# Kernel optimization log

Measured on AMD Instinct MI355X. Metric: run time of the kernel, lower is better.

## Reference

```python
import jax, jax.numpy as jnp
import numpy as np

N_NODES = 100000
N_EDGES = 1600000
F_IN, H1, H2, N_CLS = 512, 180, 120, 40
NEG_SLOPE = 0.01  # F.leaky_relu default


def setup_inputs() -> dict:
    key = jax.random.key(0)
    ks = jax.random.split(key, 8)
    x = jax.random.normal(ks[0], (N_NODES, F_IN), dtype=jnp.float32)
    edge_index = jax.random.randint(ks[1], (2, N_EDGES), 0, N_NODES, dtype=jnp.int64)
    W1 = jax.random.normal(ks[2], (F_IN, H1), dtype=jnp.float32) / np.sqrt(F_IN)
    b1 = jnp.zeros((H1,), dtype=jnp.float32)
    W2 = jax.random.normal(ks[3], (H1, H2), dtype=jnp.float32) / np.sqrt(H1)
    b2 = jnp.zeros((H2,), dtype=jnp.float32)
    W3 = jax.random.normal(ks[4], (H2, N_CLS), dtype=jnp.float32) / np.sqrt(H2)
    b3 = jnp.zeros((N_CLS,), dtype=jnp.float32)
    return {"x": x, "edge_index": edge_index, "W1": W1, "b1": b1,
            "W2": W2, "b2": b2, "W3": W3, "b3": b3}


def _add_self_loops(edge_index, n):
    loop = jnp.arange(n, dtype=edge_index.dtype)
    src = jnp.concatenate([edge_index[0], loop])
    dst = jnp.concatenate([edge_index[1], loop])
    return src, dst


def _gcn_conv(h, src, dst, norm, W, b, n):
    # PyG GCNConv: linear transform first, then normalized scatter-add at dst.
    h = h @ W  # [N, out]
    msg = norm[:, None] * h[src]  # gather at source, per-edge scale
    out = jax.ops.segment_sum(msg, dst, num_segments=n)  # scatter-add at dest
    return out + b


def reference(x, edge_index, W1, b1, W2, b2, W3, b3):
    n = x.shape[0]
    src, dst = _add_self_loops(edge_index, n)
    # symmetric normalization deg^-1/2 * deg^-1/2 on self-loop-augmented graph
    ones = jnp.ones(dst.shape[0], dtype=x.dtype)
    deg = jax.ops.segment_sum(ones, dst, num_segments=n)
    dinv = jnp.where(deg > 0, jax.lax.rsqrt(deg), 0.0)
    norm = dinv[src] * dinv[dst]  # [E+N]

    h = _gcn_conv(x, src, dst, norm, W1, b1, n)
    h = jnp.where(h >= 0, h, NEG_SLOPE * h)
    h = _gcn_conv(h, src, dst, norm, W2, b2, n)
    h = jnp.where(h >= 0, h, NEG_SLOPE * h)
    logits = h @ W3 + b3
    return jax.nn.log_softmax(logits, axis=1)
```

## Files before the change

### kernel.cpp

```cpp
#include <hip/hip_runtime.h>
#include <math.h>

typedef __attribute__((ext_vector_type(8))) short short8;
typedef __attribute__((ext_vector_type(4))) float f32x4;

static constexpr int F_IN = 512;
static constexpr int H1V = 180, H1P = 192;
static constexpr int H2V = 120, H2P = 128;
static constexpr int NC  = 40,  NCP = 64;

__device__ inline unsigned f2bf(float f) {
    unsigned u = __float_as_uint(f);
    return (u + 0x7fffu + ((u >> 16) & 1u)) >> 16;
}
__device__ inline unsigned cvtpk(float lo, float hi) {
    unsigned r;
    asm("v_cvt_pk_bf16_f32 %0, %1, %2" : "=v"(r) : "v"(lo), "v"(hi));
    return r;
}
#define BLO(u) __uint_as_float((u) << 16)
#define BHI(u) __uint_as_float((u) & 0xffff0000u)

__device__ inline void gload_lds16(const void* gsrc, void* ldst) {
    __builtin_amdgcn_global_load_lds(
        (const __attribute__((address_space(1))) void*)gsrc,
        (__attribute__((address_space(3))) void*)ldst, 16, 0, 0);
}

__global__ void k_init(const int* __restrict__ ei, int* __restrict__ flag,
                       const float* __restrict__ W1, const float* __restrict__ W2,
                       const float* __restrict__ W3, const float* __restrict__ b1,
                       const float* __restrict__ b2, const float* __restrict__ b3,
                       unsigned short* __restrict__ W1s, unsigned short* __restrict__ W2s,
                       unsigned short* __restrict__ W3s, float* __restrict__ b1p,
                       float* __restrict__ b2p, float* __restrict__ b3p) {
    if (blockIdx.x < 16) {
        int i = blockIdx.x * 256 + threadIdx.x;
        if (ei[2 * i + 1] != 0) flag[0] = 1;
        return;
    }
    const int n1 = F_IN * H1P;
    const int n2 = n1 + H1P * H2P;
    const int n3 = n2 + H2P * NCP;
    const int n4 = n3 + H1P;
    const int n5 = n4 + H2P;
    const int n6 = n5 + NCP;
    int i = (blockIdx.x - 16) * 256 + threadIdx.x;
    if (i < n1) {
        int k = i / H1P, c = i % H1P;
        float v = (c < H1V) ? W1[k * H1V + c] : 0.0f;
        W1s[(size_t)(k >> 3) * H1P * 8 + c * 8 + (k & 7)] = (unsigned short)f2bf(v);
    } else if (i < n2) {
        int j = i - n1;
        int k = j / H2P, c = j % H2P;
        float v = (k < H1V && c < H2V) ? W2[k * H2V + c] : 0.0f;
        W2s[(size_t)(k >> 3) * H2P * 8 + c * 8 + (k & 7)] = (unsigned short)f2bf(v);
    } else if (i < n3) {
        int j = i - n2;
        int k = j / NCP, c = j % NCP;
        float v = (k < H2V && c < NC) ? W3[k * NC + c] : 0.0f;
        W3s[(size_t)(k >> 3) * NCP * 8 + c * 8 + (k & 7)] = (unsigned short)f2bf(v);
    } else if (i < n4) {
        int c = i - n3;
        b1p[c] = (c < H1V) ? b1[c] : 0.0f;
    } else if (i < n5) {
        int c = i - n4;
        b2p[c] = (c < H2V) ? b2[c] : 0.0f;
    } else if (i < n6) {
        int c = i - n5;
        b3p[c] = (c < NC) ? b3[c] : -1e30f;
    }
}

__global__ void k_hist(const int* __restrict__ ei, int E, const int* __restrict__ flag,
                       int* __restrict__ deg, int* __restrict__ dst32,
                       uint2* __restrict__ sr) {
    int e = blockIdx.x * 256 + threadIdx.x;
    if (e >= E) return;
    bool i64 = (flag[0] == 0);
    int s, d;
    if (i64) { s = ei[2 * e]; d = ei[2 * E + 2 * e]; }
    else     { s = ei[e];     d = ei[E + e]; }
    int r = atomicAdd(&deg[d], 1);
    dst32[e] = d;
    sr[e] = make_uint2((unsigned)s, (unsigned)r);
}

__global__ void k_scan1(const int* __restrict__ deg, int* __restrict__ rp,
                        int* __restrict__ bsum, float* __restrict__ dinv, int n) {
    __shared__ int s[256];
    int t = threadIdx.x;
    int base = blockIdx.x * 1024 + t * 4;
    int v0 = (base + 0 < n) ? deg[base + 0] : 0;
    int v1 = (base + 1 < n) ? deg[base + 1] : 0;
    int v2 = (base + 2 < n) ? deg[base + 2] : 0;
    int v3 = (base + 3 < n) ? deg[base + 3] : 0;
    if (base + 0 < n) dinv[base + 0] = rsqrtf((float)(v0 + 1));
    if (base + 1 < n) dinv[base + 1] = rsqrtf((float)(v1 + 1));
    if (base + 2 < n) dinv[base + 2] = rsqrtf((float)(v2 + 1));
    if (base + 3 < n) dinv[base + 3] = rsqrtf((float)(v3 + 1));
    int sum = v0 + v1 + v2 + v3;
    s[t] = sum;
    __syncthreads();
    for (int off = 1; off < 256; off <<= 1) {
        int x = (t >= off) ? s[t - off] : 0;
        __syncthreads();
        s[t] += x;
        __syncthreads();
    }
    int run = s[t] - sum;
    if (t == 255) bsum[blockIdx.x] = s[255];
    if (base + 0 < n) rp[base + 0] = run; run += v0;
    if (base + 1 < n) rp[base + 1] = run; run += v1;
    if (base + 2 < n) rp[base + 2] = run; run += v2;
    if (base + 3 < n) rp[base + 3] = run;
}

__global__ void k_scan2(int* __restrict__ bsum, int nb) {
    __shared__ int s[128];
    int t = threadIdx.x;
    int v = (t < nb) ? bsum[t] : 0;
    s[t] = v;
    __syncthreads();
    for (int off = 1; off < 128; off <<= 1) {
        int x = (t >= off) ? s[t - off] : 0;
        __syncthreads();
        s[t] += x;
        __syncthreads();
    }
    if (t < nb) bsum[t] = s[t] - v;
}

__global__ void k_scan3(const int* __restrict__ bsum, int* __restrict__ rp,
                        int n, int E) {
    int i = blockIdx.x * 256 + threadIdx.x;
    if (i < n) {
        rp[i] = rp[i] + bsum[i >> 10];
    } else if (i == n) {
        rp[n] = E;
    }
}

__global__ __launch_bounds__(256) void k_fill(const int* __restrict__ dst32,
                                              const uint2* __restrict__ sr, int E,
                                              const int* __restrict__ rp,
                                              int* __restrict__ csr,
                                              int bw, int chunk) {
    int bkt = blockIdx.x & 7;
    int lo = bkt * bw, hi = lo + bw;
    int ch = blockIdx.x >> 3;
    int e0 = ch * chunk;
    int e1 = min(E, e0 + chunk);
    for (int e = e0 + (int)threadIdx.x; e < e1; e += 256) {
        int d = dst32[e];
        if (d >= lo && d < hi) {
            uint2 v = sr[e];
            csr[rp[d] + (int)v.y] = (int)v.x;
        }
    }
}

__global__ __launch_bounds__(256) void k_gemm1(const float* __restrict__ X,
                                               const short8* __restrict__ Bs,
                                               const float* __restrict__ dinv,
                                               signed char* __restrict__ Hq,
                                               float* __restrict__ sc,
                                               int M) {
    __shared__ float ldsf[6144];
    char* lds = (char*)ldsf;
    int t = threadIdx.x;
    int w = t >> 6, l = t & 63;
    int lr = l & 15, kg = l >> 4;
    int row0 = blockIdx.x * 32;
    int colb = w * 48;

    f32x4 acc[2][3];
#pragma unroll
    for (int m = 0; m < 2; ++m)
#pragma unroll
        for (int nn = 0; nn < 3; ++nn) acc[m][nn] = (f32x4){0.f, 0.f, 0.f, 0.f};

    auto stage = [&](int kb, int buf) {
#pragma unroll
        for (int j = 0; j < 2; ++j) {
            int o = j * 4096 + t * 16;
            int row = o >> 8;
            int col4 = ((o >> 4) & 15) ^ (row & 15);
            int rowg = row0 + row;
            if (rowg >= M) rowg = M - 1;
            gload_lds16(X + (size_t)rowg * F_IN + kb + col4 * 4,
                        lds + buf * 8192 + j * 4096 + w * 1024);
        }
    };

    short8 breg[2][2][3];
    auto loadB = [&](int ts, int pp) {
#pragma unroll
        for (int kk = 0; kk < 2; ++kk)
#pragma unroll
            for (int nn = 0; nn < 3; ++nn)
                breg[pp][kk][nn] =
                    Bs[(size_t)(ts * 8 + kk * 4 + kg) * H1P + colb + nn * 16 + lr];
    };

    auto compute = [&](int cur, int pp) {
#pragma unroll
        for (int kk = 0; kk < 2; ++kk) {
            short8 a[2];
#pragma unroll
            for (int m = 0; m < 2; ++m) {
                int row = m * 16 + lr;
                char* base = lds + cur * 8192 + row * 256;
                int c0 = kk * 8 + kg * 2;
                float4 v0 = *(const float4*)(base + (((c0 + 0) ^ (row & 15)) * 16));
                float4 v1 = *(const float4*)(base + (((c0 + 1) ^ (row & 15)) * 16));
                union { unsigned u[4]; short8 s; } cu;
                cu.u[0] = cvtpk(v0.x, v0.y);
                cu.u[1] = cvtpk(v0.z, v0.w);
                cu.u[2] = cvtpk(v1.x, v1.y);
                cu.u[3] = cvtpk(v1.z, v1.w);
                a[m] = cu.s;
            }
#pragma unroll
            for (int m = 0; m < 2; ++m)
#pragma unroll
                for (int nn = 0; nn < 3; ++nn)
                    acc[m][nn] = __builtin_amdgcn_mfma_f32_16x16x32_bf16(
                        a[m], breg[pp][kk][nn], acc[m][nn], 0, 0, 0);
        }
    };

    stage(0, 0);
    stage(64, 1);
    loadB(0, 0);
    asm volatile("s_waitcnt vmcnt(8)" ::: "memory");
    __builtin_amdgcn_s_barrier();
    __builtin_amdgcn_sched_barrier(0);

#pragma unroll
    for (int ts = 0; ts < 8; ++ts) {
        if (ts < 6) stage((ts + 2) * 64, (ts + 2) % 3);
        if (ts < 7) loadB(ts + 1, (ts + 1) & 1);
        compute(ts % 3, ts & 1);
        if (ts < 7) {
            if (ts < 6) {
                asm volatile("s_waitcnt vmcnt(8)" ::: "memory");
            } else {
                asm volatile("s_waitcnt vmcnt(6)" ::: "memory");
            }
            __builtin_amdgcn_s_barrier();
            __builtin_amdgcn_sched_barrier(0);
        }
    }

    __syncthreads();
    float* rmaxp = (float*)lds;
#pragma unroll
    for (int m = 0; m < 2; ++m) {
#pragma unroll
        for (int j = 0; j < 4; ++j) {
            int rl = m * 16 + kg * 4 + j;
            int grow = row0 + rl;
            float dv = (grow < M) ? dinv[grow] : 0.f;
            float lm = 0.f;
#pragma unroll
            for (int nn = 0; nn < 3; ++nn)
                lm = fmaxf(lm, fabsf(acc[m][nn][j] * dv));
#pragma unroll
            for (int d = 1; d < 16; d <<= 1)
                lm = fmaxf(lm, __shfl_xor(lm, d));
            if (lr == 0) rmaxp[rl * 4 + w] = lm;
        }
    }
    __syncthreads();
#pragma unroll
    for (int m = 0; m < 2; ++m) {
#pragma unroll
        for (int j = 0; j < 4; ++j) {
            int rl = m * 16 + kg * 4 + j;
            int grow = row0 + rl;
            if (grow >= M) continue;
            float dv = dinv[grow];
            float rm = fmaxf(fmaxf(rmaxp[rl * 4 + 0], rmaxp[rl * 4 + 1]),
                             fmaxf(rmaxp[rl * 4 + 2], rmaxp[rl * 4 + 3]));
            float inv = (rm > 0.f) ? 127.0f / rm : 0.f;
            if (w == 0 && lr == 0) sc[grow] = rm * (1.0f / 127.0f);
#pragma unroll
            for (int nn = 0; nn < 3; ++nn) {
                float v = acc[m][nn][j] * dv * inv;
                v = fminf(fmaxf(rintf(v), -127.f), 127.f);
                Hq[(size_t)grow * H1P + colb + nn * 16 + lr] = (signed char)(int)v;
            }
        }
    }
}

__global__ __launch_bounds__(256) void k_gat1q(const signed char* __restrict__ Hq,
                                               const float* __restrict__ sc,
                                               const float* __restrict__ dinv,
                                               const int* __restrict__ rp,
                                               const int* __restrict__ csr,
                                               const float* __restrict__ bias,
                                               uint2* __restrict__ out, int n) {
    int wv = threadIdx.x >> 6, l = threadIdx.x & 63;
    int i = blockIdx.x * 4 + wv;
    if (i >= n) return;
    bool act = l < 48;
    int c = act ? l : 0;
    const unsigned* Hr = (const unsigned*)(Hq + c * 4);

    float a0, a1, a2, a3;
    {
        unsigned w0 = Hr[(size_t)i * 48];
        float s0 = sc[i];
        a0 = (float)(signed char)(w0) * s0;
        a1 = (float)(signed char)(w0 >> 8) * s0;
        a2 = (float)(signed char)(w0 >> 16) * s0;
        a3 = (float)(signed char)(w0 >> 24) * s0;
    }
    float p0 = 0.f, p1 = 0.f, p2 = 0.f, p3 = 0.f;

    int e0 = rp[i], e1 = rp[i + 1];
    int e = e0;
    for (; e + 7 < e1; e += 8) {
        int s[8];
#pragma unroll
        for (int q = 0; q < 8; ++q) s[q] = csr[e + q];
        float scs[8];
#pragma unroll
        for (int q = 0; q < 8; ++q) scs[q] = sc[s[q]];
        unsigned v[8];
#pragma unroll
        for (int q = 0; q < 8; ++q) v[q] = Hr[(size_t)s[q] * 48];
#pragma unroll
        for (int q = 0; q < 8; q += 2) {
            a0 = fmaf((float)(signed char)(v[q]), scs[q], a0);
            a1 = fmaf((float)(signed char)(v[q] >> 8), scs[q], a1);
            a2 = fmaf((float)(signed char)(v[q] >> 16), scs[q], a2);
            a3 = fmaf((float)(signed char)(v[q] >> 24), scs[q], a3);
            p0 = fmaf((float)(signed char)(v[q + 1]), scs[q + 1], p0);
            p1 = fmaf((float)(signed char)(v[q + 1] >> 8), scs[q + 1], p1);
            p2 = fmaf((float)(signed char)(v[q + 1] >> 16), scs[q + 1], p2);
            p3 = fmaf((float)(signed char)(v[q + 1] >> 24), scs[q + 1], p3);
        }
    }
    for (; e < e1; ++e) {
        int s0 = csr[e];
        float sq = sc[s0];
        unsigned w0 = Hr[(size_t)s0 * 48];
        a0 = fmaf((float)(signed char)(w0), sq, a0);
        a1 = fmaf((float)(signed char)(w0 >> 8), sq, a1);
        a2 = fmaf((float)(signed char)(w0 >> 16), sq, a2);
        a3 = fmaf((float)(signed char)(w0 >> 24), sq, a3);
    }
    a0 += p0; a1 += p1; a2 += p2; a3 += p3;

    float di = dinv[i];
    float4 bb = *(const float4*)(bias + 4 * c);
    float o0 = fmaf(di, a0, bb.x);
    float o1 = fmaf(di, a1, bb.y);
    float o2 = fmaf(di, a2, bb.z);
    float o3 = fmaf(di, a3, bb.w);
    o0 = o0 >= 0.f ? o0 : 0.01f * o0;
    o1 = o1 >= 0.f ? o1 : 0.01f * o1;
    o2 = o2 >= 0.f ? o2 : 0.01f * o2;
    o3 = o3 >= 0.f ? o3 : 0.01f * o3;
    if (act) {
        uint2 r;
        r.x = (f2bf(o1) << 16) | f2bf(o0);
        r.y = (f2bf(o3) << 16) | f2bf(o2);
        out[(size_t)i * 48 + c] = r;
    }
}

__global__ __launch_bounds__(512) void k_gemm2(const unsigned short* __restrict__ A,
                                               const short8* __restrict__ Bs,
                                               const float* __restrict__ dinv,
                                               unsigned short* __restrict__ Hout,
                                               int M) {
    __shared__ unsigned short ldsu[16384];
    char* lds = (char*)ldsu;
    int t = threadIdx.x;
    int w = t >> 6, l = t & 63;
    int lr = l & 15, kg = l >> 4;
    int wr = w >> 2, wc = w & 3;
    int row0 = blockIdx.x * 128;
    int colb = wc * 32;

    f32x4 acc[4][2];
#pragma unroll
    for (int m = 0; m < 4; ++m)
#pragma unroll
        for (int nn = 0; nn < 2; ++nn) acc[m][nn] = (f32x4){0.f, 0.f, 0.f, 0.f};

    auto stage = [&](int kb, int buf) {
#pragma unroll
        for (int j = 0; j < 2; ++j) {
            int o = j * 8192 + t * 16;
            int row = o >> 7;
            int chunk = ((o >> 4) & 7) ^ (row & 7);
            int rowg = row0 + row;
            if (rowg >= M) rowg = M - 1;
            gload_lds16(A + (size_t)rowg * H1P + kb + chunk * 8,
                        lds + buf * 16384 + j * 8192 + w * 1024);
        }
    };

    stage(0, 0);
    __syncthreads();

    for (int ts = 0; ts < 3; ++ts) {
        int cur = ts & 1;
        if (ts < 2) stage((ts + 1) * 64, cur ^ 1);
        short8 b[2][2];
#pragma unroll
        for (int kk = 0; kk < 2; ++kk)
#pragma unroll
            for (int nn = 0; nn < 2; ++nn)
                b[kk][nn] = Bs[(size_t)(ts * 8 + kk * 4 + kg) * H2P + colb + nn * 16 + lr];
        short8 a[2][4];
#pragma unroll
        for (int kk = 0; kk < 2; ++kk)
#pragma unroll
            for (int m = 0; m < 4; ++m) {
                int row = wr * 64 + m * 16 + lr;
                a[kk][m] = *(const short8*)(lds + cur * 16384 + row * 128 +
                                            (((kk * 4 + kg) ^ (row & 7)) * 16));
            }
#pragma unroll
        for (int kk = 0; kk < 2; ++kk)
#pragma unroll
            for (int m = 0; m < 4; ++m)
#pragma unroll
                for (int nn = 0; nn < 2; ++nn)
                    acc[m][nn] = __builtin_amdgcn_mfma_f32_16x16x32_bf16(a[kk][m], b[kk][nn], acc[m][nn], 0, 0, 0);
        __syncthreads();
    }

#pragma unroll
    for (int m = 0; m < 4; ++m) {
        int r4 = row0 + wr * 64 + m * 16 + kg * 4;
#pragma unroll
        for (int j = 0; j < 4; ++j) {
            int grow = r4 + j;
            if (grow < M) {
                float dv = dinv[grow];
#pragma unroll
                for (int nn = 0; nn < 2; ++nn)
                    Hout[(size_t)grow * H2P + colb + nn * 16 + lr] =
                        (unsigned short)f2bf(acc[m][nn][j] * dv);
            }
        }
    }
}

__global__ __launch_bounds__(256) void k_gat2(const uint2* __restrict__ H,
                                              const float* __restrict__ dinv,
                                              const int* __restrict__ rp,
                                              const int* __restrict__ csr,
                                              const float* __restrict__ bias,
                                              uint2* __restrict__ out, int n) {
    int wv = threadIdx.x >> 6, l = threadIdx.x & 63;
    int half = l >> 5, c = l & 31;
    int i = blockIdx.x * 8 + wv * 2 + half;
    if (i >= n) return;
    const uint2* Hr = H + c;

    float a0, a1, a2, a3;
    {
        uint2 v = Hr[(size_t)i * 32];
        a0 = BLO(v.x); a1 = BHI(v.x); a2 = BLO(v.y); a3 = BHI(v.y);
    }
    float p0 = 0.f, p1 = 0.f, p2 = 0.f, p3 = 0.f;

    int e0 = rp[i], e1 = rp[i + 1];
    int e = e0;
    for (; e + 7 < e1; e += 8) {
        int s[8];
#pragma unroll
        for (int q = 0; q < 8; ++q) s[q] = csr[e + q];
        uint2 v[8];
#pragma unroll
        for (int q = 0; q < 8; ++q) v[q] = Hr[(size_t)s[q] * 32];
#pragma unroll
        for (int q = 0; q < 8; q += 2) {
            a0 += BLO(v[q].x); a1 += BHI(v[q].x); a2 += BLO(v[q].y); a3 += BHI(v[q].y);
            p0 += BLO(v[q + 1].x); p1 += BHI(v[q + 1].x); p2 += BLO(v[q + 1].y); p3 += BHI(v[q + 1].y);
        }
    }
    for (; e + 3 < e1; e += 4) {
        int s0 = csr[e], s1 = csr[e + 1], s2 = csr[e + 2], s3 = csr[e + 3];
        uint2 va = Hr[(size_t)s0 * 32];
        uint2 vb = Hr[(size_t)s1 * 32];
        uint2 vc = Hr[(size_t)s2 * 32];
        uint2 vd = Hr[(size_t)s3 * 32];
        a0 += BLO(va.x); a1 += BHI(va.x); a2 += BLO(va.y); a3 += BHI(va.y);
        p0 += BLO(vb.x); p1 += BHI(vb.x); p2 += BLO(vb.y); p3 += BHI(vb.y);
        a0 += BLO(vc.x); a1 += BHI(vc.x); a2 += BLO(vc.y); a3 += BHI(vc.y);
        p0 += BLO(vd.x); p1 += BHI(vd.x); p2 += BLO(vd.y); p3 += BHI(vd.y);
    }
    for (; e < e1; ++e) {
        int s0 = csr[e];
        uint2 va = Hr[(size_t)s0 * 32];
        a0 += BLO(va.x); a1 += BHI(va.x); a2 += BLO(va.y); a3 += BHI(va.y);
    }
    a0 += p0; a1 += p1; a2 += p2; a3 += p3;

    float di = dinv[i];
    float4 bb = *(const float4*)(bias + 4 * c);
    float o0 = fmaf(di, a0, bb.x);
    float o1 = fmaf(di, a1, bb.y);
    float o2 = fmaf(di, a2, bb.z);
    float o3 = fmaf(di, a3, bb.w);
    o0 = o0 >= 0.f ? o0 : 0.01f * o0;
    o1 = o1 >= 0.f ? o1 : 0.01f * o1;
    o2 = o2 >= 0.f ? o2 : 0.01f * o2;
    o3 = o3 >= 0.f ? o3 : 0.01f * o3;
    uint2 r;
    r.x = (f2bf(o1) << 16) | f2bf(o0);
    r.y = (f2bf(o3) << 16) | f2bf(o2);
    out[(size_t)i * 32 + c] = r;
}

__global__ __launch_bounds__(256) void k_out(const unsigned short* __restrict__ H,
                                             const short8* __restrict__ Bs,
                                             const float* __restrict__ b3p,
                                             float* __restrict__ out, int M) {
    int t = threadIdx.x;
    int w = t >> 6, l = t & 63;
    int lr = l & 15, kg = l >> 4;
    int row0 = blockIdx.x * 64 + w * 16;

    f32x4 acc[4];
#pragma unroll
    for (int f = 0; f < 4; ++f) acc[f] = (f32x4){0.f, 0.f, 0.f, 0.f};

    int rowa = row0 + lr;
    if (rowa >= M) rowa = M - 1;
    const unsigned short* arow = H + (size_t)rowa * H2P;

#pragma unroll
    for (int ks = 0; ks < 4; ++ks) {
        short8 a = *(const short8*)(arow + ks * 32 + kg * 8);
#pragma unroll
        for (int f = 0; f < 4; ++f) {
            short8 b = Bs[(size_t)(ks * 4 + kg) * NCP + f * 16 + lr];
            acc[f] = __builtin_amdgcn_mfma_f32_16x16x32_bf16(a, b, acc[f], 0, 0, 0);
        }
    }

    float bl[4];
#pragma unroll
    for (int f = 0; f < 4; ++f) bl[f] = b3p[f * 16 + lr];

#pragma unroll
    for (int j = 0; j < 4; ++j) {
        int grow = row0 + kg * 4 + j;
        float lg[4];
#pragma unroll
        for (int f = 0; f < 4; ++f) lg[f] = acc[f][j] + bl[f];
        float m = fmaxf(fmaxf(lg[0], lg[1]), fmaxf(lg[2], lg[3]));
#pragma unroll
        for (int d = 1; d < 16; d <<= 1) m = fmaxf(m, __shfl_xor(m, d));
        float s = expf(lg[0] - m) + expf(lg[1] - m) + expf(lg[2] - m) + expf(lg[3] - m);
#pragma unroll
        for (int d = 1; d < 16; d <<= 1) s += __shfl_xor(s, d);
        float lse = m + logf(s);
        if (grow < M) {
#pragma unroll
            for (int f = 0; f < 4; ++f) {
                int c = f * 16 + lr;
                if (c < NC) out[(size_t)grow * NC + c] = lg[f] - lse;
            }
        }
    }
}

extern "C" void kernel_launch(void* const* d_in, const int* in_sizes, int n_in,
                              void* d_out, int out_size, void* d_ws, size_t ws_size,
                              hipStream_t stream) {
    const float* x  = (const float*)d_in[0];
    const int*   ei = (const int*)d_in[1];
    const float* W1 = (const float*)d_in[2];
    const float* b1 = (const float*)d_in[3];
    const float* W2 = (const float*)d_in[4];
    const float* b2 = (const float*)d_in[5];
    const float* W3 = (const float*)d_in[6];
    const float* b3 = (const float*)d_in[7];
    float* outp = (float*)d_out;

    int n = in_sizes[0] / F_IN;
    int E = in_sizes[1] / 2;

    char* p = (char*)d_ws;
    auto alloc = [&](size_t bytes) -> char* {
        char* r = p;
        p += (bytes + 511) & ~(size_t)511;
        return r;
    };
    int*            fd     = (int*)alloc((size_t)(n + 1) * 4);
    int*            flag   = fd;
    int*            deg    = fd + 1;
    float*          dinv   = (float*)alloc((size_t)n * 4);
    int*            rp     = (int*)alloc((size_t)(n + 1) * 4);
    int*            bsum   = (int*)alloc(4096);
    int*            dst32  = (int*)alloc((size_t)E * 4);
    uint2*          sr     = (uint2*)alloc((size_t)E * 8);
    int*            csr    = (int*)alloc((size_t)E * 4);
    unsigned short* W1s    = (unsigned short*)alloc((size_t)F_IN * H1P * 2);
    unsigned short* W2s    = (unsigned short*)alloc((size_t)H1P * H2P * 2);
    unsigned short* W3s    = (unsigned short*)alloc((size_t)H2P * NCP * 2);
    float*          b1p    = (float*)alloc(H1P * 4);
    float*          b2p    = (float*)alloc(H2P * 4);
    float*          b3p    = (float*)alloc(NCP * 4);
    signed char*    h1q    = (signed char*)alloc((size_t)n * H1P);
    float*          sc     = (float*)alloc((size_t)n * 4);
    unsigned short* h1agg  = (unsigned short*)alloc((size_t)n * H1P * 2);
    unsigned short* h2     = (unsigned short*)alloc((size_t)n * H2P * 2);
    unsigned short* h2agg  = (unsigned short*)alloc((size_t)n * H2P * 2);

    hipMemsetAsync(fd, 0, (size_t)(n + 1) * 4, stream);

    k_init<<<530, 256, 0, stream>>>(ei, flag, W1, W2, W3, b1, b2, b3,
                                    W1s, W2s, W3s, b1p, b2p, b3p);

    int eb = (E + 255) / 256;
    k_hist<<<eb, 256, 0, stream>>>(ei, E, flag, deg, dst32, sr);

    int nb = (n + 1023) / 1024;
    k_scan1<<<nb, 256, 0, stream>>>(deg, rp, bsum, dinv, n);
    k_scan2<<<1, 128, 0, stream>>>(bsum, nb);
    k_scan3<<<(n + 1 + 255) / 256, 256, 0, stream>>>(bsum, rp, n, E);

    int bw = (n + 7) / 8;
    int nch = 256;
    int chunk = (E + nch - 1) / nch;
    k_fill<<<nch * 8, 256, 0, stream>>>(dst32, sr, E, rp, csr, bw, chunk);

    k_gemm1<<<(n + 31) / 32, 256, 0, stream>>>(x, (const short8*)W1s, dinv, h1q, sc, n);
    k_gat1q<<<(n + 3) / 4, 256, 0, stream>>>(h1q, sc, dinv, rp, csr, b1p,
                                             (uint2*)h1agg, n);
    k_gemm2<<<(n + 127) / 128, 512, 0, stream>>>(h1agg, (const short8*)W2s, dinv, h2, n);
    k_gat2<<<(n + 7) / 8, 256, 0, stream>>>((const uint2*)h2, dinv, rp, csr, b2p,
                                            (uint2*)h2agg, n);
    k_out<<<(n + 63) / 64, 256, 0, stream>>>(h2agg, (const short8*)W3s, b3p, outp, n);
}
```

Before: 362.2 us.

## Fuse edge histogram with first GEMM in one interleaved launch

The degree histogram / edge-packing kernel and the first GEMM+int8 quantization kernel now run in a single launch, with blocks interleaved so the memory-bound atomic histogram overlaps the MFMA GEMM. Removing the GEMM's dependency on dinv means the per-row quantization scale is computed without degree normalization, and dinv is folded into a new scd array in the scan kernel. This lets the two independent phases share the GPU concurrently and drops one launch, at the cost of an extra n-sized scale array and slightly different quantization (the scale is taken before the dinv multiply).

```diff
diff --git a/kernel.cpp b/kernel.cpp
--- a/kernel.cpp
+++ b/kernel.cpp
@@ -72,22 +72,170 @@
     }
 }
 
-__global__ void k_hist(const int* __restrict__ ei, int E, const int* __restrict__ flag,
-                       int* __restrict__ deg, int* __restrict__ dst32,
-                       uint2* __restrict__ sr) {
-    int e = blockIdx.x * 256 + threadIdx.x;
-    if (e >= E) return;
-    bool i64 = (flag[0] == 0);
-    int s, d;
-    if (i64) { s = ei[2 * e]; d = ei[2 * E + 2 * e]; }
-    else     { s = ei[e];     d = ei[E + e]; }
-    int r = atomicAdd(&deg[d], 1);
-    dst32[e] = d;
-    sr[e] = make_uint2((unsigned)s, (unsigned)r);
+__global__ __launch_bounds__(256) void k_megaA(const float* __restrict__ X,
+                                               const short8* __restrict__ Bs,
+                                               signed char* __restrict__ Hq,
+                                               float* __restrict__ sc, int M, int gb,
+                                               const int* __restrict__ ei, int E,
+                                               const int* __restrict__ flag,
+                                               int* __restrict__ deg,
+                                               int* __restrict__ dst32,
+                                               uint2* __restrict__ sr,
+                                               int interleave) {
+    __shared__ float ldsf[6144];
+    int bid;
+    bool isGemm;
+    if (interleave) {
+        int g = blockIdx.x / 3, r = blockIdx.x % 3;
+        if (r == 0) { isGemm = true; bid = g; }
+        else        { isGemm = false; bid = g * 2 + r - 1; }
+    } else {
+        isGemm = (int)blockIdx.x < gb;
+        bid = isGemm ? blockIdx.x : blockIdx.x - gb;
+    }
+
+    if (!isGemm) {
+        int e = bid * 256 + threadIdx.x;
+        if (e >= E) return;
+        bool i64 = (flag[0] == 0);
+        int s, d;
+        if (i64) { s = ei[2 * e]; d = ei[2 * E + 2 * e]; }
+        else     { s = ei[e];     d = ei[E + e]; }
+        int r = atomicAdd(&deg[d], 1);
+        dst32[e] = d;
+        sr[e] = make_uint2((unsigned)s, (unsigned)r);
+        return;
+    }
+
+    char* lds = (char*)ldsf;
+    int t = threadIdx.x;
+    int w = t >> 6, l = t & 63;
+    int lr = l & 15, kg = l >> 4;
+    int row0 = bid * 32;
+    int colb = w * 48;
+
+    f32x4 acc[2][3];
+#pragma unroll
+    for (int m = 0; m < 2; ++m)
+#pragma unroll
+        for (int nn = 0; nn < 3; ++nn) acc[m][nn] = (f32x4){0.f, 0.f, 0.f, 0.f};
+
+    auto stage = [&](int kb, int buf) {
+#pragma unroll
+        for (int j = 0; j < 2; ++j) {
+            int o = j * 4096 + t * 16;
+            int row = o >> 8;
+            int col4 = ((o >> 4) & 15) ^ (row & 15);
+            int rowg = row0 + row;
+            if (rowg >= M) rowg = M - 1;
+            gload_lds16(X + (size_t)rowg * F_IN + kb + col4 * 4,
+                        lds + buf * 8192 + j * 4096 + w * 1024);
+        }
+    };
+
+    short8 breg[2][2][3];
+    auto loadB = [&](int ts, int pp) {
+#pragma unroll
+        for (int kk = 0; kk < 2; ++kk)
+#pragma unroll
+            for (int nn = 0; nn < 3; ++nn)
+                breg[pp][kk][nn] =
+                    Bs[(size_t)(ts * 8 + kk * 4 + kg) * H1P + colb + nn * 16 + lr];
+    };
+
+    auto compute = [&](int cur, int pp) {
+#pragma unroll
+        for (int kk = 0; kk < 2; ++kk) {
+            short8 a[2];
+#pragma unroll
+            for (int m = 0; m < 2; ++m) {
+                int row = m * 16 + lr;
+                char* base = lds + cur * 8192 + row * 256;
+                int c0 = kk * 8 + kg * 2;
+                float4 v0 = *(const float4*)(base + (((c0 + 0) ^ (row & 15)) * 16));
+                float4 v1 = *(const float4*)(base + (((c0 + 1) ^ (row & 15)) * 16));
+                union { unsigned u[4]; short8 s; } cu;
+                cu.u[0] = cvtpk(v0.x, v0.y);
+                cu.u[1] = cvtpk(v0.z, v0.w);
+                cu.u[2] = cvtpk(v1.x, v1.y);
+                cu.u[3] = cvtpk(v1.z, v1.w);
+                a[m] = cu.s;
+            }
+#pragma unroll
+            for (int m = 0; m < 2; ++m)
+#pragma unroll
+                for (int nn = 0; nn < 3; ++nn)
+                    acc[m][nn] = __builtin_amdgcn_mfma_f32_16x16x32_bf16(
+                        a[m], breg[pp][kk][nn], acc[m][nn], 0, 0, 0);
+        }
+    };
+
+    stage(0, 0);
+    stage(64, 1);
+    loadB(0, 0);
+    asm volatile("s_waitcnt vmcnt(8)" ::: "memory");
+    __builtin_amdgcn_s_barrier();
+    __builtin_amdgcn_sched_barrier(0);
+
+#pragma unroll
+    for (int ts = 0; ts < 8; ++ts) {
+        if (ts < 6) stage((ts + 2) * 64, (ts + 2) % 3);
+        if (ts < 7) loadB(ts + 1, (ts + 1) & 1);
+        compute(ts % 3, ts & 1);
+        if (ts < 7) {
+            if (ts < 6) {
+                asm volatile("s_waitcnt vmcnt(8)" ::: "memory");
+            } else {
+                asm volatile("s_waitcnt vmcnt(6)" ::: "memory");
+            }
+            __builtin_amdgcn_s_barrier();
+            __builtin_amdgcn_sched_barrier(0);
+        }
+    }
+
+    __syncthreads();
+    float* rmaxp = (float*)lds;
+#pragma unroll
+    for (int m = 0; m < 2; ++m) {
+#pragma unroll
+        for (int j = 0; j < 4; ++j) {
+            int rl = m * 16 + kg * 4 + j;
+            float lm = 0.f;
+#pragma unroll
+            for (int nn = 0; nn < 3; ++nn)
+                lm = fmaxf(lm, fabsf(acc[m][nn][j]));
+#pragma unroll
+            for (int d = 1; d < 16; d <<= 1)
+                lm = fmaxf(lm, __shfl_xor(lm, d));
+            if (lr == 0) rmaxp[rl * 4 + w] = lm;
+        }
+    }
+    __syncthreads();
+#pragma unroll
+    for (int m = 0; m < 2; ++m) {
+#pragma unroll
+        for (int j = 0; j < 4; ++j) {
+            int rl = m * 16 + kg * 4 + j;
+            int grow = row0 + rl;
+            if (grow >= M) continue;
+            float rm = fmaxf(fmaxf(rmaxp[rl * 4 + 0], rmaxp[rl * 4 + 1]),
+                             fmaxf(rmaxp[rl * 4 + 2], rmaxp[rl * 4 + 3]));
+            float inv = (rm > 0.f) ? 127.0f / rm : 0.f;
+            if (w == 0 && lr == 0) sc[grow] = rm * (1.0f / 127.0f);
+#pragma unroll
+            for (int nn = 0; nn < 3; ++nn) {
+                float v = acc[m][nn][j] * inv;
+                v = fminf(fmaxf(rintf(v), -127.f), 127.f);
+                Hq[(size_t)grow * H1P + colb + nn * 16 + lr] = (signed char)(int)v;
+            }
+        }
+    }
 }
 
 __global__ void k_scan1(const int* __restrict__ deg, int* __restrict__ rp,
-                        int* __restrict__ bsum, float* __restrict__ dinv, int n) {
+                        int* __restrict__ bsum, float* __restrict__ dinv,
+                        const float* __restrict__ sc, float* __restrict__ scd,
+                        int n) {
     __shared__ int s[256];
     int t = threadIdx.x;
     int base = blockIdx.x * 1024 + t * 4;
@@ -95,10 +243,10 @@
     int v1 = (base + 1 < n) ? deg[base + 1] : 0;
     int v2 = (base + 2 < n) ? deg[base + 2] : 0;
     int v3 = (base + 3 < n) ? deg[base + 3] : 0;
-    if (base + 0 < n) dinv[base + 0] = rsqrtf((float)(v0 + 1));
-    if (base + 1 < n) dinv[base + 1] = rsqrtf((float)(v1 + 1));
-    if (base + 2 < n) dinv[base + 2] = rsqrtf((float)(v2 + 1));
-    if (base + 3 < n) dinv[base + 3] = rsqrtf((float)(v3 + 1));
+    if (base + 0 < n) { float d = rsqrtf((float)(v0 + 1)); dinv[base + 0] = d; scd[base + 0] = d * sc[base + 0]; }
+    if (base + 1 < n) { float d = rsqrtf((float)(v1 + 1)); dinv[base + 1] = d; scd[base + 1] = d * sc[base + 1]; }
+    if (base + 2 < n) { float d = rsqrtf((float)(v2 + 1)); dinv[base + 2] = d; scd[base + 2] = d * sc[base + 2]; }
+    if (base + 3 < n) { float d = rsqrtf((float)(v3 + 1)); dinv[base + 3] = d; scd[base + 3] = d * sc[base + 3]; }
     int sum = v0 + v1 + v2 + v3;
     s[t] = sum;
     __syncthreads();
@@ -160,143 +308,8 @@
     }
 }
 
-__global__ __launch_bounds__(256) void k_gemm1(const float* __restrict__ X,
-                                               const short8* __restrict__ Bs,
-                                               const float* __restrict__ dinv,
-                                               signed char* __restrict__ Hq,
-                                               float* __restrict__ sc,
-                                               int M) {
-    __shared__ float ldsf[6144];
-    char* lds = (char*)ldsf;
-    int t = threadIdx.x;
-    int w = t >> 6, l = t & 63;
-    int lr = l & 15, kg = l >> 4;
-    int row0 = blockIdx.x * 32;
-    int colb = w * 48;
-
-    f32x4 acc[2][3];
-#pragma unroll
-    for (int m = 0; m < 2; ++m)
-#pragma unroll
-        for (int nn = 0; nn < 3; ++nn) acc[m][nn] = (f32x4){0.f, 0.f, 0.f, 0.f};
-
-    auto stage = [&](int kb, int buf) {
-#pragma unroll
-        for (int j = 0; j < 2; ++j) {
-            int o = j * 4096 + t * 16;
-            int row = o >> 8;
-            int col4 = ((o >> 4) & 15) ^ (row & 15);
-            int rowg = row0 + row;
-            if (rowg >= M) rowg = M - 1;
-            gload_lds16(X + (size_t)rowg * F_IN + kb + col4 * 4,
-                        lds + buf * 8192 + j * 4096 + w * 1024);
-        }
-    };
-
-    short8 breg[2][2][3];
-    auto loadB = [&](int ts, int pp) {
-#pragma unroll
-        for (int kk = 0; kk < 2; ++kk)
-#pragma unroll
-            for (int nn = 0; nn < 3; ++nn)
-                breg[pp][kk][nn] =
-                    Bs[(size_t)(ts * 8 + kk * 4 + kg) * H1P + colb + nn * 16 + lr];
-    };
-
-    auto compute = [&](int cur, int pp) {
-#pragma unroll
-        for (int kk = 0; kk < 2; ++kk) {
-            short8 a[2];
-#pragma unroll
-            for (int m = 0; m < 2; ++m) {
-                int row = m * 16 + lr;
-                char* base = lds + cur * 8192 + row * 256;
-                int c0 = kk * 8 + kg * 2;
-                float4 v0 = *(const float4*)(base + (((c0 + 0) ^ (row & 15)) * 16));
-                float4 v1 = *(const float4*)(base + (((c0 + 1) ^ (row & 15)) * 16));
-                union { unsigned u[4]; short8 s; } cu;
-                cu.u[0] = cvtpk(v0.x, v0.y);
-                cu.u[1] = cvtpk(v0.z, v0.w);
-                cu.u[2] = cvtpk(v1.x, v1.y);
-                cu.u[3] = cvtpk(v1.z, v1.w);
-                a[m] = cu.s;
-            }
-#pragma unroll
-            for (int m = 0; m < 2; ++m)
-#pragma unroll
-                for (int nn = 0; nn < 3; ++nn)
-                    acc[m][nn] = __builtin_amdgcn_mfma_f32_16x16x32_bf16(
-                        a[m], breg[pp][kk][nn], acc[m][nn], 0, 0, 0);
-        }
-    };
-
-    stage(0, 0);
-    stage(64, 1);
-    loadB(0, 0);
-    asm volatile("s_waitcnt vmcnt(8)" ::: "memory");
-    __builtin_amdgcn_s_barrier();
-    __builtin_amdgcn_sched_barrier(0);
-
-#pragma unroll
-    for (int ts = 0; ts < 8; ++ts) {
-        if (ts < 6) stage((ts + 2) * 64, (ts + 2) % 3);
-        if (ts < 7) loadB(ts + 1, (ts + 1) & 1);
-        compute(ts % 3, ts & 1);
-        if (ts < 7) {
-            if (ts < 6) {
-                asm volatile("s_waitcnt vmcnt(8)" ::: "memory");
-            } else {
-                asm volatile("s_waitcnt vmcnt(6)" ::: "memory");
-            }
-            __builtin_amdgcn_s_barrier();
-            __builtin_amdgcn_sched_barrier(0);
-        }
-    }
-
-    __syncthreads();
-    float* rmaxp = (float*)lds;
-#pragma unroll
-    for (int m = 0; m < 2; ++m) {
-#pragma unroll
-        for (int j = 0; j < 4; ++j) {
-            int rl = m * 16 + kg * 4 + j;
-            int grow = row0 + rl;
-            float dv = (grow < M) ? dinv[grow] : 0.f;
-            float lm = 0.f;
-#pragma unroll
-            for (int nn = 0; nn < 3; ++nn)
-                lm = fmaxf(lm, fabsf(acc[m][nn][j] * dv));
-#pragma unroll
-            for (int d = 1; d < 16; d <<= 1)
-                lm = fmaxf(lm, __shfl_xor(lm, d));
-            if (lr == 0) rmaxp[rl * 4 + w] = lm;
-        }
-    }
-    __syncthreads();
-#pragma unroll
-    for (int m = 0; m < 2; ++m) {
-#pragma unroll
-        for (int j = 0; j < 4; ++j) {
-            int rl = m * 16 + kg * 4 + j;
-            int grow = row0 + rl;
-            if (grow >= M) continue;
-            float dv = dinv[grow];
-            float rm = fmaxf(fmaxf(rmaxp[rl * 4 + 0], rmaxp[rl * 4 + 1]),
-                             fmaxf(rmaxp[rl * 4 + 2], rmaxp[rl * 4 + 3]));
-            float inv = (rm > 0.f) ? 127.0f / rm : 0.f;
-            if (w == 0 && lr == 0) sc[grow] = rm * (1.0f / 127.0f);
-#pragma unroll
-            for (int nn = 0; nn < 3; ++nn) {
-                float v = acc[m][nn][j] * dv * inv;
-                v = fminf(fmaxf(rintf(v), -127.f), 127.f);
-                Hq[(size_t)grow * H1P + colb + nn * 16 + lr] = (signed char)(int)v;
-            }
-        }
-    }
-}
-
 __global__ __launch_bounds__(256) void k_gat1q(const signed char* __restrict__ Hq,
-                                               const float* __restrict__ sc,
+                                               const float* __restrict__ scd,
                                                const float* __restrict__ dinv,
                                                const int* __restrict__ rp,
                                                const int* __restrict__ csr,
@@ -312,7 +325,7 @@
     float a0, a1, a2, a3;
     {
         unsigned w0 = Hr[(size_t)i * 48];
-        float s0 = sc[i];
+        float s0 = scd[i];
         a0 = (float)(signed char)(w0) * s0;
         a1 = (float)(signed char)(w0 >> 8) * s0;
         a2 = (float)(signed char)(w0 >> 16) * s0;
@@ -328,7 +341,7 @@
         for (int q = 0; q < 8; ++q) s[q] = csr[e + q];
         float scs[8];
 #pragma unroll
-        for (int q = 0; q < 8; ++q) scs[q] = sc[s[q]];
+        for (int q = 0; q < 8; ++q) scs[q] = scd[s[q]];
         unsigned v[8];
 #pragma unroll
         for (int q = 0; q < 8; ++q) v[q] = Hr[(size_t)s[q] * 48];
@@ -346,7 +359,7 @@
     }
     for (; e < e1; ++e) {
         int s0 = csr[e];
-        float sq = sc[s0];
+        float sq = scd[s0];
         unsigned w0 = Hr[(size_t)s0 * 48];
         a0 = fmaf((float)(signed char)(w0), sq, a0);
         a1 = fmaf((float)(signed char)(w0 >> 8), sq, a1);
@@ -615,6 +628,7 @@
     float*          b3p    = (float*)alloc(NCP * 4);
     signed char*    h1q    = (signed char*)alloc((size_t)n * H1P);
     float*          sc     = (float*)alloc((size_t)n * 4);
+    float*          scd    = (float*)alloc((size_t)n * 4);
     unsigned short* h1agg  = (unsigned short*)alloc((size_t)n * H1P * 2);
     unsigned short* h2     = (unsigned short*)alloc((size_t)n * H2P * 2);
     unsigned short* h2agg  = (unsigned short*)alloc((size_t)n * H2P * 2);
@@ -624,11 +638,14 @@
     k_init<<<530, 256, 0, stream>>>(ei, flag, W1, W2, W3, b1, b2, b3,
                                     W1s, W2s, W3s, b1p, b2p, b3p);
 
+    int gb = (n + 31) / 32;
     int eb = (E + 255) / 256;
-    k_hist<<<eb, 256, 0, stream>>>(ei, E, flag, deg, dst32, sr);
+    int interleave = (eb == 2 * gb) ? 1 : 0;
+    k_megaA<<<gb + eb, 256, 0, stream>>>(x, (const short8*)W1s, h1q, sc, n, gb,
+                                         ei, E, flag, deg, dst32, sr, interleave);
 
     int nb = (n + 1023) / 1024;
-    k_scan1<<<nb, 256, 0, stream>>>(deg, rp, bsum, dinv, n);
+    k_scan1<<<nb, 256, 0, stream>>>(deg, rp, bsum, dinv, sc, scd, n);
     k_scan2<<<1, 128, 0, stream>>>(bsum, nb);
     k_scan3<<<(n + 1 + 255) / 256, 256, 0, stream>>>(bsum, rp, n, E);
 
@@ -637,8 +654,7 @@
     int chunk = (E + nch - 1) / nch;
     k_fill<<<nch * 8, 256, 0, stream>>>(dst32, sr, E, rp, csr, bw, chunk);
 
-    k_gemm1<<<(n + 31) / 32, 256, 0, stream>>>(x, (const short8*)W1s, dinv, h1q, sc, n);
-    k_gat1q<<<(n + 3) / 4, 256, 0, stream>>>(h1q, sc, dinv, rp, csr, b1p,
+    k_gat1q<<<(n + 3) / 4, 256, 0, stream>>>(h1q, scd, dinv, rp, csr, b1p,
                                              (uint2*)h1agg, n);
     k_gemm2<<<(n + 127) / 128, 512, 0, stream>>>(h1agg, (const short8*)W2s, dinv, h2, n);
     k_gat2<<<(n + 7) / 8, 256, 0, stream>>>((const uint2*)h2, dinv, rp, csr, b2p,
```

Result: faster. 317.5 us (-12.3%).
